# Kernel optimization log

Hardware: AMD Instinct MI355X
Metric: run time of the kernel (lower is better)

Reference implementation:

```python
import jax, jax.numpy as jnp
import numpy as np

B, N, D, H = 16, 1024, 768, 12
HD = D // H
SCALE = HD ** -0.5


def setup_inputs() -> dict:
    key = jax.random.key(0)
    ks = jax.random.split(key, 7)
    s = D ** -0.5  # keep activations well-scaled
    return {
        "x": jax.random.normal(ks[0], (B, N, D), dtype=jnp.float32),
        "Wq": jax.random.normal(ks[1], (D, D), dtype=jnp.float32) * s,
        "bq": jax.random.normal(ks[2], (D,), dtype=jnp.float32) * 0.01,
        "Wk": jax.random.normal(ks[3], (D, D), dtype=jnp.float32) * s,
        "bk": jax.random.normal(ks[4], (D,), dtype=jnp.float32) * 0.01,
        "Wp": jax.random.normal(ks[5], (D, D), dtype=jnp.float32) * s,
        "bp": jax.random.normal(ks[6], (D,), dtype=jnp.float32) * 0.01,
    }


def reference(x, Wq, bq, Wk, bk, Wp, bp):
    # Faithful to source: V uses the K projection (bug in original, Vm unused).
    q = x @ Wq.T + bq  # [B,N,D]
    k = x @ Wk.T + bk
    v = k              # V = Km(x) in the original code
    # split heads -> [B,H,N,HD]
    q = q.reshape(B, N, H, HD).transpose(0, 2, 1, 3)
    k = k.reshape(B, N, H, HD).transpose(0, 2, 1, 3)
    v = v.reshape(B, N, H, HD).transpose(0, 2, 1, 3)
    scores = jnp.einsum("bhqd,bhkd->bhqk", q, k) * SCALE  # [B,H,N,N]
    attn = jax.nn.softmax(scores, axis=-1)
    out = jnp.einsum("bhqk,bhkd->bhqd", attn, v)  # [B,H,N,HD]
    out = out.transpose(0, 2, 1, 3).reshape(B, N, D)
    return out @ Wp.T + bp
```

## Files before the change

### kernel.cpp

```cpp
#include <hip/hip_runtime.h>
#include <hip/hip_bf16.h>


#define DEV static __device__ __forceinline__

typedef __attribute__((ext_vector_type(8)))  short  short8;
typedef __attribute__((ext_vector_type(4)))  short  short4v;
typedef __attribute__((ext_vector_type(4)))  float  f32x4;
typedef __attribute__((ext_vector_type(16))) float  f32x16;
typedef __attribute__((ext_vector_type(4)))  unsigned short ushort4v;
typedef __attribute__((ext_vector_type(4)))  unsigned int   u32x4;

DEV unsigned short f2bf(float x) {
  unsigned int u = __float_as_uint(x);
  u = u + 0x7fffu + ((u >> 16) & 1u);
  return (unsigned short)(u >> 16);
}

#define GLOAD_LDS16(g, l)                                                     \
  __builtin_amdgcn_global_load_lds(                                           \
      (const __attribute__((address_space(1))) void*)(g),                     \
      (__attribute__((address_space(3))) void*)(l), 16, 0, 0)

__global__ __launch_bounds__(256) void k_cvt(const float* __restrict__ src,
                                             unsigned short* __restrict__ dst,
                                             int n4) {
  int i = blockIdx.x * 256 + threadIdx.x;
  if (i >= n4) return;
  f32x4 v = *(const f32x4*)(src + (size_t)i * 4);
  ushort4v o;
  o[0] = f2bf(v[0]); o[1] = f2bf(v[1]); o[2] = f2bf(v[2]); o[3] = f2bf(v[3]);
  *(ushort4v*)(dst + (size_t)i * 4) = o;
}

__global__ __launch_bounds__(256) void k_stackbias(const float* __restrict__ bq,
                                                   const float* __restrict__ bk,
                                                   float* __restrict__ bqk) {
  int i = blockIdx.x * 256 + threadIdx.x;
  if (i < 768) bqk[i] = bq[i];
  else if (i < 1536) bqk[i] = bk[i - 768];
}

template <int MODE>
__global__ __launch_bounds__(256) void k_gemm_bt(const unsigned short* __restrict__ A,
                                                 const unsigned short* __restrict__ W,
                                                 const float* __restrict__ bias,
                                                 void* __restrict__ Cv,
                                                 int M, int N, int K) {
  __shared__ char lds[32768];
  char* ldsA = lds;
  char* ldsB = lds + 16384;
  const int tid  = threadIdx.x;
  const int wid  = tid >> 6;
  const int lane = tid & 63;
  const int row0 = blockIdx.x * 128;
  const int col0 = blockIdx.y * 128;
  const int wr = (wid >> 1) * 64;
  const int wc = (wid & 1) * 64;
  const int lr = lane & 15;
  const int lg = lane >> 4;

  f32x4 acc[4][4];
#pragma unroll
  for (int m = 0; m < 4; ++m)
#pragma unroll
    for (int n = 0; n < 4; ++n)
#pragma unroll
      for (int r = 0; r < 4; ++r) acc[m][n][r] = 0.f;

  for (int kt = 0; kt < K; kt += 64) {
    __syncthreads();
#pragma unroll
    for (int p = 0; p < 4; ++p) {
      int blkbase = (p * 4 + wid);
      int chunk = blkbase * 64 + lane;
      int r  = chunk >> 3;
      int cb = ((chunk & 7) << 4) ^ ((r & 7) << 4);
      const char* ga = (const char*)(A + (size_t)(row0 + r) * K + kt) + cb;
      GLOAD_LDS16(ga, ldsA + blkbase * 1024);
      const char* gb = (const char*)(W + (size_t)(col0 + r) * K + kt) + cb;
      GLOAD_LDS16(gb, ldsB + blkbase * 1024);
    }
    asm volatile("s_waitcnt vmcnt(0)" ::: "memory");
    __syncthreads();
#pragma unroll
    for (int kk = 0; kk < 2; ++kk) {
      short8 af[4], bf[4];
#pragma unroll
      for (int m = 0; m < 4; ++m) {
        int row = wr + m * 16 + lr;
        int a   = row * 128 + ((kk * 64 + lg * 16) ^ ((row & 7) << 4));
        af[m] = *(const short8*)(ldsA + a);
        int col = wc + m * 16 + lr;
        int b   = col * 128 + ((kk * 64 + lg * 16) ^ ((col & 7) << 4));
        bf[m] = *(const short8*)(ldsB + b);
      }
#pragma unroll
      for (int m = 0; m < 4; ++m)
#pragma unroll
        for (int n = 0; n < 4; ++n)
          acc[m][n] = __builtin_amdgcn_mfma_f32_16x16x32_bf16(af[m], bf[n], acc[m][n], 0, 0, 0);
    }
  }

  const int r0g = row0 + wr + lg * 4;
  const int c0g = col0 + wc + lr;
  float bv[4];
#pragma unroll
  for (int n = 0; n < 4; ++n) bv[n] = bias[c0g + n * 16];

  if constexpr (MODE == 2) {
    const bool kh = (col0 >= 768);
    unsigned short* dst = (unsigned short*)Cv + (kh ? ((size_t)16384 * 768 - 768) : 0);
    const float sc = kh ? 1.0f : 0.125f;
#pragma unroll
    for (int m = 0; m < 4; ++m)
#pragma unroll
      for (int n = 0; n < 4; ++n)
#pragma unroll
        for (int r = 0; r < 4; ++r) {
          float v = (acc[m][n][r] + bv[n]) * sc;
          dst[(size_t)(r0g + m * 16 + r) * 768 + (c0g + n * 16)] = f2bf(v);
        }
  } else {
#pragma unroll
    for (int m = 0; m < 4; ++m)
#pragma unroll
      for (int n = 0; n < 4; ++n)
#pragma unroll
        for (int r = 0; r < 4; ++r) {
          float v = acc[m][n][r] + bv[n];
          ((float*)Cv)[(size_t)(r0g + m * 16 + r) * N + (c0g + n * 16)] = v;
        }
  }
}

__global__ __launch_bounds__(256) void k_transpose(const unsigned short* __restrict__ kin,
                                                   unsigned short* __restrict__ kT2) {
  __shared__ unsigned short t[64][72];
  const int bh = blockIdx.x;
  const int h = bh % 12, b = bh / 12;
  const int n0 = blockIdx.y * 64;
  const int tid = threadIdx.x;
#pragma unroll
  for (int p = 0; p < 2; ++p) {
    int c = p * 256 + tid;
    int i = c >> 3, jc = c & 7;
    short8 v = *(const short8*)(kin + (size_t)(b * 1024 + n0 + i) * 768 + h * 64 + jc * 8);
    *(short8*)(&t[i][jc * 8]) = v;
  }
  __syncthreads();
#pragma unroll
  for (int p = 0; p < 2; ++p) {
    int c = p * 256 + tid;
    int hd = c >> 3, nc = c & 7;
    short8 v;
#pragma unroll
    for (int j = 0; j < 8; ++j) v[j] = (short)t[nc * 8 + j][hd];
    int tile = (n0 >> 5) + (nc >> 2);
    int kloc = (nc & 3) * 8;
    *(short8*)(kT2 + (((size_t)bh * 32 + tile) * 64 + hd) * 32 + kloc) = v;
  }
}

__global__ __launch_bounds__(256) void k_attn(const unsigned short* __restrict__ qg,
                                              const unsigned short* __restrict__ kg,
                                              const unsigned short* __restrict__ kT2,
                                              unsigned short* __restrict__ og) {
  __shared__ char lds[18432];
  const int tid  = threadIdx.x;
  const int w    = tid >> 6;
  const int lane = tid & 63;
  const int q32  = lane & 31;
  const int hi   = lane >> 5;
  const int blk  = (blockIdx.x & 7) * 192 + (blockIdx.x >> 3);
  const int qc   = blk & 7;
  const int bh   = blk >> 3;
  const int h = bh % 12, b = bh / 12;
  const int qbase = qc * 128 + w * 32;

  const unsigned short* Qp = qg + (size_t)(b * 1024 + qbase + q32) * 768 + h * 64;
  short8 qf[4];
#pragma unroll
  for (int c = 0; c < 4; ++c) qf[c] = *(const short8*)(Qp + c * 16 + hi * 8);

  const int sr = tid >> 3, sp = tid & 7;
  const unsigned short* ksrc = kg + (size_t)(b * 1024 + sr) * 768 + h * 64 + ((sp ^ (sr & 7)) << 3);
  const int vh = tid >> 2, vp = tid & 3;
  const unsigned short* vsrc = kT2 + (size_t)bh * 65536 + (size_t)vh * 32 + ((vp ^ ((vh >> 1) & 3)) << 3);

  float mrow = -__builtin_inff();
  float lsum = 0.f;
  f32x16 o0, o1;
#pragma unroll
  for (int r = 0; r < 16; ++r) { o0[r] = 0.f; o1[r] = 0.f; }

  GLOAD_LDS16(ksrc, lds + tid * 16);
  GLOAD_LDS16(vsrc, lds + 4096 + tid * 16);

  const int kfo0 = q32 * 128;
  const int vswz = (q32 >> 1) & 3;

  for (int t = 0; t < 32; ++t) {
    const int bo = (t & 1) << 13;
    asm volatile("s_waitcnt vmcnt(0)" ::: "memory");
    __syncthreads();
    if (t + 1 < 32) {
      const int bn = ((t + 1) & 1) << 13;
      GLOAD_LDS16(ksrc + (size_t)(t + 1) * 24576, lds + bn + tid * 16);
      GLOAD_LDS16(vsrc + (size_t)(t + 1) * 2048, lds + bn + 4096 + tid * 16);
    }

    f32x16 s;
#pragma unroll
    for (int r = 0; r < 16; ++r) s[r] = 0.f;
#pragma unroll
    for (int c = 0; c < 4; ++c) {
      short8 kf = *(const short8*)(lds + bo + kfo0 + (((c * 2 + hi) ^ (q32 & 7)) << 4));
      s = __builtin_amdgcn_mfma_f32_32x32x16_bf16(kf, qf[c], s, 0, 0, 0);
    }

    short8 vf[2][2];
#pragma unroll
    for (int f = 0; f < 2; ++f)
#pragma unroll
      for (int s2 = 0; s2 < 2; ++s2)
        vf[s2][f] = *(const short8*)(lds + bo + 4096 + (f * 32 + q32) * 64 +
                                     (((s2 * 2 + hi) ^ vswz) << 4));

    float tmax = s[0];
#pragma unroll
    for (int r = 1; r < 16; ++r) tmax = fmaxf(tmax, s[r]);
    tmax = fmaxf(tmax, __shfl_xor(tmax, 32));
    if (!__all(tmax <= mrow + 8.f)) {
      float mnew = fmaxf(mrow, tmax);
      float corr = __expf(mrow - mnew);
      lsum *= corr;
#pragma unroll
      for (int r = 0; r < 16; ++r) { o0[r] *= corr; o1[r] *= corr; }
      mrow = mnew;
    }
    float p[16], ps = 0.f;
#pragma unroll
    for (int r = 0; r < 16; ++r) { p[r] = __expf(s[r] - mrow); ps += p[r]; }
    ps += __shfl_xor(ps, 32);
    lsum += ps;

    unsigned pw[8];
#pragma unroll
    for (int i = 0; i < 8; ++i)
      asm("v_cvt_pk_bf16_f32 %0, %1, %2" : "=v"(pw[i]) : "v"(p[2 * i]), "v"(p[2 * i + 1]));

    {
      unsigned x0 = pw[0], y0 = pw[2], x1 = pw[1], y1 = pw[3];
      asm("v_permlane32_swap_b32 %0, %1" : "+v"(x0), "+v"(y0));
      asm("v_permlane32_swap_b32 %0, %1" : "+v"(x1), "+v"(y1));
      union { u32x4 wv; short8 sv; } u;
      u.wv[0] = x0; u.wv[1] = x1; u.wv[2] = y0; u.wv[3] = y1;
      o0 = __builtin_amdgcn_mfma_f32_32x32x16_bf16(vf[0][0], u.sv, o0, 0, 0, 0);
      o1 = __builtin_amdgcn_mfma_f32_32x32x16_bf16(vf[0][1], u.sv, o1, 0, 0, 0);
    }
    {
      unsigned x0 = pw[4], y0 = pw[6], x1 = pw[5], y1 = pw[7];
      asm("v_permlane32_swap_b32 %0, %1" : "+v"(x0), "+v"(y0));
      asm("v_permlane32_swap_b32 %0, %1" : "+v"(x1), "+v"(y1));
      union { u32x4 wv; short8 sv; } u;
      u.wv[0] = x0; u.wv[1] = x1; u.wv[2] = y0; u.wv[3] = y1;
      o0 = __builtin_amdgcn_mfma_f32_32x32x16_bf16(vf[1][0], u.sv, o0, 0, 0, 0);
      o1 = __builtin_amdgcn_mfma_f32_32x32x16_bf16(vf[1][1], u.sv, o1, 0, 0, 0);
    }
  }

  __syncthreads();
  float inv = 1.f / lsum;
  char* lw = lds + w * 4608;
#pragma unroll
  for (int mg = 0; mg < 4; ++mg) {
    short4v t;
#pragma unroll
    for (int i = 0; i < 4; ++i) t[i] = (short)f2bf(o0[mg * 4 + i] * inv);
    *(short4v*)(lw + q32 * 144 + mg * 16 + hi * 8) = t;
#pragma unroll
    for (int i = 0; i < 4; ++i) t[i] = (short)f2bf(o1[mg * 4 + i] * inv);
    *(short4v*)(lw + q32 * 144 + 64 + mg * 16 + hi * 8) = t;
  }
  __syncthreads();
  const size_t obase = (size_t)(b * 1024 + qbase) * 768 + h * 64;
#pragma unroll
  for (int pp = 0; pp < 4; ++pp) {
    int chunk = pp * 64 + lane;
    int qr = chunk >> 3, cc = chunk & 7;
    short8 v = *(const short8*)(lw + qr * 144 + cc * 16);
    *(short8*)(og + obase + (size_t)qr * 768 + cc * 8) = v;
  }
}

extern "C" void kernel_launch(void* const* d_in, const int* in_sizes, int n_in,
                              void* d_out, int out_size, void* d_ws, size_t ws_size,
                              hipStream_t stream) {
  const float* x  = (const float*)d_in[0];
  const float* Wq = (const float*)d_in[1];
  const float* bq = (const float*)d_in[2];
  const float* Wk = (const float*)d_in[3];
  const float* bk = (const float*)d_in[4];
  const float* Wp = (const float*)d_in[5];
  const float* bp = (const float*)d_in[6];
  float* out = (float*)d_out;
  char* ws = (char*)d_ws;

  const size_t XB = (size_t)16384 * 768 * 2;
  const size_t WB = (size_t)768 * 768 * 2;
  if (ws_size < 3 * XB + 3 * WB + 6144) return;

  unsigned short* xb  = (unsigned short*)(ws);
  unsigned short* qb  = (unsigned short*)(ws + XB);
  unsigned short* kb  = (unsigned short*)(ws + 2 * XB);
  unsigned short* wqb = (unsigned short*)(ws + 3 * XB);
  unsigned short* wkb = (unsigned short*)(ws + 3 * XB + WB);
  unsigned short* wpb = (unsigned short*)(ws + 3 * XB + 2 * WB);
  float*          bqk = (float*)(ws + 3 * XB + 3 * WB);
  unsigned short* ab  = xb;
  unsigned short* kTb = (unsigned short*)d_out;

  k_cvt<<<12288, 256, 0, stream>>>(x, xb, 16384 * 768 / 4);
  k_cvt<<<576, 256, 0, stream>>>(Wq, wqb, 768 * 768 / 4);
  k_cvt<<<576, 256, 0, stream>>>(Wk, wkb, 768 * 768 / 4);
  k_cvt<<<576, 256, 0, stream>>>(Wp, wpb, 768 * 768 / 4);
  k_stackbias<<<6, 256, 0, stream>>>(bq, bk, bqk);

  k_gemm_bt<2><<<dim3(128, 12), 256, 0, stream>>>(xb, wqb, bqk, qb, 16384, 1536, 768);
  k_transpose<<<dim3(192, 16), 256, 0, stream>>>(kb, kTb);
  k_attn<<<1536, 256, 0, stream>>>(qb, kb, kTb, ab);
  k_gemm_bt<0><<<dim3(128, 6), 256, 0, stream>>>(ab, wpb, bp, out, 16384, 768, 768);
}
```

Measured before the change: 185.9 us.

## Fuse K transpose into QK GEMM epilogue, merge prep kernels, use exp2

The QK projection GEMM epilogue now writes the transposed K tile layout directly, which removes the separate transpose kernel and its re-read of K. The three weight conversions and the bias stacking are merged into one launch. The attention softmax folds log2(e) into the Q scale and uses the native v_exp_f32 instruction, with the rescale threshold widened to match the base-2 domain. In exchange the GEMM epilogue takes on extra scattered 8-byte stores.

```diff
diff --git a/kernel.cpp b/kernel.cpp
--- a/kernel.cpp
+++ b/kernel.cpp
@@ -11,10 +11,18 @@
 typedef __attribute__((ext_vector_type(4)))  unsigned short ushort4v;
 typedef __attribute__((ext_vector_type(4)))  unsigned int   u32x4;
 
+#define QSCALE 0.180336880f
+
 DEV unsigned short f2bf(float x) {
   unsigned int u = __float_as_uint(x);
   u = u + 0x7fffu + ((u >> 16) & 1u);
   return (unsigned short)(u >> 16);
+}
+
+DEV float exp2v(float x) {
+  float r;
+  asm("v_exp_f32 %0, %1" : "=v"(r) : "v"(x));
+  return r;
 }
 
 #define GLOAD_LDS16(g, l)                                                     \
@@ -33,12 +41,29 @@
   *(ushort4v*)(dst + (size_t)i * 4) = o;
 }
 
-__global__ __launch_bounds__(256) void k_stackbias(const float* __restrict__ bq,
-                                                   const float* __restrict__ bk,
-                                                   float* __restrict__ bqk) {
-  int i = blockIdx.x * 256 + threadIdx.x;
-  if (i < 768) bqk[i] = bq[i];
-  else if (i < 1536) bqk[i] = bk[i - 768];
+__global__ __launch_bounds__(256) void k_prep(const float* __restrict__ Wq,
+                                              const float* __restrict__ Wk,
+                                              const float* __restrict__ Wp,
+                                              const float* __restrict__ bq,
+                                              const float* __restrict__ bk,
+                                              unsigned short* __restrict__ wqb,
+                                              unsigned short* __restrict__ wkb,
+                                              unsigned short* __restrict__ wpb,
+                                              float* __restrict__ bqk) {
+  int blk = blockIdx.x;
+  if (blk < 1728) {
+    const float* src = (blk < 576) ? Wq : (blk < 1152) ? Wk : Wp;
+    unsigned short* dst = (blk < 576) ? wqb : (blk < 1152) ? wkb : wpb;
+    int i = (blk % 576) * 256 + threadIdx.x;
+    f32x4 v = *(const f32x4*)(src + (size_t)i * 4);
+    ushort4v o;
+    o[0] = f2bf(v[0]); o[1] = f2bf(v[1]); o[2] = f2bf(v[2]); o[3] = f2bf(v[3]);
+    *(ushort4v*)(dst + (size_t)i * 4) = o;
+  } else {
+    int i = (blk - 1728) * 256 + threadIdx.x;
+    if (i < 768) bqk[i] = bq[i];
+    else if (i < 1536) bqk[i] = bk[i - 768];
+  }
 }
 
 template <int MODE>
@@ -46,6 +71,7 @@
                                                  const unsigned short* __restrict__ W,
                                                  const float* __restrict__ bias,
                                                  void* __restrict__ Cv,
+                                                 unsigned short* __restrict__ kT2g,
                                                  int M, int N, int K) {
   __shared__ char lds[32768];
   char* ldsA = lds;
@@ -112,16 +138,28 @@
   if constexpr (MODE == 2) {
     const bool kh = (col0 >= 768);
     unsigned short* dst = (unsigned short*)Cv + (kh ? ((size_t)16384 * 768 - 768) : 0);
-    const float sc = kh ? 1.0f : 0.125f;
+    const float sc = kh ? 1.0f : QSCALE;
 #pragma unroll
     for (int m = 0; m < 4; ++m)
 #pragma unroll
-      for (int n = 0; n < 4; ++n)
+      for (int n = 0; n < 4; ++n) {
+        ushort4v t4;
 #pragma unroll
         for (int r = 0; r < 4; ++r) {
           float v = (acc[m][n][r] + bv[n]) * sc;
-          dst[(size_t)(r0g + m * 16 + r) * 768 + (c0g + n * 16)] = f2bf(v);
+          unsigned short bfv = f2bf(v);
+          dst[(size_t)(r0g + m * 16 + r) * 768 + (c0g + n * 16)] = bfv;
+          t4[r] = bfv;
         }
+        if (kh) {
+          int hd2  = c0g + n * 16 - 768;
+          int rowb = r0g + m * 16;
+          int b_ = rowb >> 10, nn = rowb & 1023;
+          size_t kbase = ((((size_t)(b_ * 12 + (hd2 >> 6)) * 32 + (nn >> 5)) * 64
+                           + (hd2 & 63)) * 32 + (nn & 31));
+          *(ushort4v*)(kT2g + kbase) = t4;
+        }
+      }
   } else {
 #pragma unroll
     for (int m = 0; m < 4; ++m)
@@ -132,34 +170,6 @@
           float v = acc[m][n][r] + bv[n];
           ((float*)Cv)[(size_t)(r0g + m * 16 + r) * N + (c0g + n * 16)] = v;
         }
-  }
-}
-
-__global__ __launch_bounds__(256) void k_transpose(const unsigned short* __restrict__ kin,
-                                                   unsigned short* __restrict__ kT2) {
-  __shared__ unsigned short t[64][72];
-  const int bh = blockIdx.x;
-  const int h = bh % 12, b = bh / 12;
-  const int n0 = blockIdx.y * 64;
-  const int tid = threadIdx.x;
-#pragma unroll
-  for (int p = 0; p < 2; ++p) {
-    int c = p * 256 + tid;
-    int i = c >> 3, jc = c & 7;
-    short8 v = *(const short8*)(kin + (size_t)(b * 1024 + n0 + i) * 768 + h * 64 + jc * 8);
-    *(short8*)(&t[i][jc * 8]) = v;
-  }
-  __syncthreads();
-#pragma unroll
-  for (int p = 0; p < 2; ++p) {
-    int c = p * 256 + tid;
-    int hd = c >> 3, nc = c & 7;
-    short8 v;
-#pragma unroll
-    for (int j = 0; j < 8; ++j) v[j] = (short)t[nc * 8 + j][hd];
-    int tile = (n0 >> 5) + (nc >> 2);
-    int kloc = (nc & 3) * 8;
-    *(short8*)(kT2 + (((size_t)bh * 32 + tile) * 64 + hd) * 32 + kloc) = v;
   }
 }
 
@@ -232,9 +242,9 @@
 #pragma unroll
     for (int r = 1; r < 16; ++r) tmax = fmaxf(tmax, s[r]);
     tmax = fmaxf(tmax, __shfl_xor(tmax, 32));
-    if (!__all(tmax <= mrow + 8.f)) {
+    if (!__all(tmax <= mrow + 11.5f)) {
       float mnew = fmaxf(mrow, tmax);
-      float corr = __expf(mrow - mnew);
+      float corr = exp2v(mrow - mnew);
       lsum *= corr;
 #pragma unroll
       for (int r = 0; r < 16; ++r) { o0[r] *= corr; o1[r] *= corr; }
@@ -242,7 +252,7 @@
     }
     float p[16], ps = 0.f;
 #pragma unroll
-    for (int r = 0; r < 16; ++r) { p[r] = __expf(s[r] - mrow); ps += p[r]; }
+    for (int r = 0; r < 16; ++r) { p[r] = exp2v(s[r] - mrow); ps += p[r]; }
     ps += __shfl_xor(ps, 32);
     lsum += ps;
 
@@ -321,15 +331,12 @@
   float*          bqk = (float*)(ws + 3 * XB + 3 * WB);
   unsigned short* ab  = xb;
   unsigned short* kTb = (unsigned short*)d_out;
+  (void)kb;
 
   k_cvt<<<12288, 256, 0, stream>>>(x, xb, 16384 * 768 / 4);
-  k_cvt<<<576, 256, 0, stream>>>(Wq, wqb, 768 * 768 / 4);
-  k_cvt<<<576, 256, 0, stream>>>(Wk, wkb, 768 * 768 / 4);
-  k_cvt<<<576, 256, 0, stream>>>(Wp, wpb, 768 * 768 / 4);
-  k_stackbias<<<6, 256, 0, stream>>>(bq, bk, bqk);
-
-  k_gemm_bt<2><<<dim3(128, 12), 256, 0, stream>>>(xb, wqb, bqk, qb, 16384, 1536, 768);
-  k_transpose<<<dim3(192, 16), 256, 0, stream>>>(kb, kTb);
+  k_prep<<<1734, 256, 0, stream>>>(Wq, Wk, Wp, bq, bk, wqb, wkb, wpb, bqk);
+
+  k_gemm_bt<2><<<dim3(128, 12), 256, 0, stream>>>(xb, wqb, bqk, qb, kTb, 16384, 1536, 768);
   k_attn<<<1536, 256, 0, stream>>>(qb, kb, kTb, ab);
-  k_gemm_bt<0><<<dim3(128, 6), 256, 0, stream>>>(ab, wpb, bp, out, 16384, 768, 768);
-}
+  k_gemm_bt<0><<<dim3(128, 6), 256, 0, stream>>>(ab, wpb, bp, out, nullptr, 16384, 768, 768);
+}
```

After: 171.5 us. 7.7% less time.
